# Optimization experiments

Measured on AMD Instinct MI355X. Metric: run time of the kernel, lower is better.

The kernel has to match this reference:

```python
import jax, jax.numpy as jnp
import numpy as np
import math

B, N, DIM, H, D = 2, 2048, 1024, 16, 64
EXPECTED_K = 1.0
LAYERSCALE_INIT = 0.001
EPS = 1e-6  # flax LayerNorm default


def layer_norm(x, scale, bias):
    mu = jnp.mean(x, axis=-1, keepdims=True)
    var = jnp.mean((x - mu) ** 2, axis=-1, keepdims=True)
    return (x - mu) * jax.lax.rsqrt(var + EPS) * scale + bias


def setup_inputs() -> dict:
    key = jax.random.key(0)
    ks = jax.random.split(key, 8)
    s = DIM ** -0.5
    x = jax.random.normal(ks[0], (B, N, DIM), jnp.float32)
    Wq = jax.random.normal(ks[1], (DIM, H * D), jnp.float32) * s
    Wk = jax.random.normal(ks[2], (DIM, H * D), jnp.float32) * s
    Wv = jax.random.normal(ks[3], (DIM, H * D), jnp.float32) * s
    Wo = jax.random.normal(ks[4], (H * D, DIM), jnp.float32) * ((H * D) ** -0.5)
    e = EXPECTED_K / N
    init_bias = jnp.full((1, 1, 1, 1), math.log(e / (1.0 - e)), jnp.float32)
    return {
        'x': x,
        'Wq': Wq, 'bq': jnp.zeros((H * D,), jnp.float32),
        'Wk': Wk, 'bk': jnp.zeros((H * D,), jnp.float32),
        'Wv': Wv, 'bv': jnp.zeros((H * D,), jnp.float32),
        'qn_scale': jnp.ones((D,), jnp.float32), 'qn_bias': jnp.zeros((D,), jnp.float32),
        'kn_scale': jnp.ones((D,), jnp.float32), 'kn_bias': jnp.zeros((D,), jnp.float32),
        'init_bias': init_bias,
        'Wo': Wo, 'bo': jnp.zeros((DIM,), jnp.float32),
        'gamma': jnp.full((DIM,), LAYERSCALE_INIT, jnp.float32),
    }


def reference(x, Wq, bq, Wk, bk, Wv, bv, qn_scale, qn_bias, kn_scale, kn_bias,
              init_bias, Wo, bo, gamma):
    Bv, Nv, _ = x.shape
    q = (x @ Wq + bq).reshape(Bv, Nv, H, D)
    k = (x @ Wk + bk).reshape(Bv, Nv, H, D)
    v = (x @ Wv + bv).reshape(Bv, Nv, H, D)
    q = layer_norm(q, qn_scale, qn_bias)
    k = layer_norm(k, kn_scale, kn_bias)
    q = jnp.swapaxes(q, 1, 2)  # [B,H,N,D]
    k = jnp.swapaxes(k, 1, 2)
    v = jnp.swapaxes(v, 1, 2)
    # NOTE: original code computes scale = head_dim**-0.5 but never applies it.
    attn_logits = jnp.einsum('bhid,bhjd->bhij', q, k)
    attn_weights = jax.nn.sigmoid(attn_logits + init_bias)
    out = jnp.einsum('bhij,bhjd->bhid', attn_weights, v)
    out = jnp.swapaxes(out, 1, 2).reshape(Bv, Nv, H * D)
    out = out @ Wo + bo
    return out * gamma
```

## Files before the change

kernel.cpp:

```cpp
#include <hip/hip_runtime.h>

#define DEV static __device__ __forceinline__

typedef __bf16 bf16x8 __attribute__((ext_vector_type(8)));
typedef __bf16 bf16x4 __attribute__((ext_vector_type(4)));
typedef float f32x4 __attribute__((ext_vector_type(4)));
typedef float f32x16 __attribute__((ext_vector_type(16)));
typedef unsigned int uint4v __attribute__((ext_vector_type(4)));
typedef unsigned short ushort4v __attribute__((ext_vector_type(4)));
using u16 = unsigned short;

#define NN 2048
#define DIMD 1024

DEV u16 f2bf(float f) {
    __bf16 b = (__bf16)f;
    return __builtin_bit_cast(u16, b);
}
DEV float bf2f(u16 s) {
    unsigned u = ((unsigned)s) << 16;
    return __builtin_bit_cast(float, u);
}
DEV bf16x8 load16(const u16* p) { return __builtin_bit_cast(bf16x8, *(const uint4v*)p); }
DEV f32x4 mfma16(bf16x8 a, bf16x8 b, f32x4 c) {
    return __builtin_amdgcn_mfma_f32_16x16x32_bf16(a, b, c, 0, 0, 0);
}
DEV f32x16 mfma32(bf16x8 a, bf16x8 b, f32x16 c) {
    return __builtin_amdgcn_mfma_f32_32x32x16_bf16(a, b, c, 0, 0, 0);
}
DEV void gl_lds16(const u16* g, u16* l) {
    __builtin_amdgcn_global_load_lds((const __attribute__((address_space(1))) void*)g,
                                     (__attribute__((address_space(3))) void*)l, 16, 0, 0);
}


__global__ __launch_bounds__(256) void k_prep(const float* __restrict__ x,
                                              const float* __restrict__ s0,
                                              const float* __restrict__ s1,
                                              const float* __restrict__ s2,
                                              const float* __restrict__ s3,
                                              u16* __restrict__ xb,
                                              u16* __restrict__ wqkv_t,
                                              u16* __restrict__ wo_t) {
    __shared__ float tile[32][33];
    const int z = blockIdx.z;
    if (z < 4) {
        const float* src = (z == 0) ? s0 : (z == 1) ? s1 : (z == 2) ? s2 : s3;
        u16* dst = (z < 3) ? (wqkv_t + (size_t)z * 1024 * 1024) : wo_t;
        int tx = threadIdx.x & 31, ty = threadIdx.x >> 5;
        int kb = blockIdx.y * 32, nb = blockIdx.x * 32;
#pragma unroll
        for (int j = 0; j < 4; ++j)
            tile[ty + 8 * j][tx] = src[(size_t)(kb + ty + 8 * j) * 1024 + nb + tx];
        __syncthreads();
#pragma unroll
        for (int j = 0; j < 4; ++j)
            dst[(size_t)(nb + ty + 8 * j) * 1024 + kb + tx] = f2bf(tile[tx][ty + 8 * j]);
    } else {
        const int bidx = blockIdx.y * 32 + blockIdx.x;
#pragma unroll
        for (int q = 0; q < 4; ++q) {
            int i = bidx * 1024 + q * 256 + threadIdx.x;
            float4 v = ((const float4*)x)[i];
            ushort4v o;
            o[0] = f2bf(v.x); o[1] = f2bf(v.y); o[2] = f2bf(v.z); o[3] = f2bf(v.w);
            *(ushort4v*)(xb + (size_t)i * 4) = o;
        }
    }
}

__global__ __launch_bounds__(256) void k_gemm_qkv(const u16* __restrict__ A,
                                                  const u16* __restrict__ Bt,
                                                  const float* __restrict__ bq,
                                                  const float* __restrict__ bk,
                                                  const float* __restrict__ bv,
                                                  const float* __restrict__ qs,
                                                  const float* __restrict__ qb,
                                                  const float* __restrict__ ks,
                                                  const float* __restrict__ kb_,
                                                  u16* __restrict__ Qf,
                                                  u16* __restrict__ Kf,
                                                  u16* __restrict__ Vf) {
    __shared__ u16 As[128 * 32];
    __shared__ u16 Bs[128 * 32];
    const int K = 1024;
    const int m0 = blockIdx.x * 128, n0 = blockIdx.y * 128;
    const int tid = threadIdx.x;
    const int lane = tid & 63, w = tid >> 6;
    const int wr = w >> 1, wc = w & 1;
    const int li = lane & 15, g = lane >> 4;

    f32x4 acc[4][4] = {};

    const u16* gA = A + (size_t)(m0 + w * 16 + (lane >> 2)) * K + (lane & 3) * 8;
    const u16* gB = Bt + (size_t)(n0 + w * 16 + (lane >> 2)) * K + (lane & 3) * 8;
    u16* lA = &As[(w * 16) * 32];
    u16* lB = &Bs[(w * 16) * 32];

    for (int k0 = 0; k0 < K; k0 += 32) {
        __syncthreads();
        gl_lds16(gA + k0, lA);
        gl_lds16(gA + (size_t)64 * K + k0, lA + 64 * 32);
        gl_lds16(gB + k0, lB);
        gl_lds16(gB + (size_t)64 * K + k0, lB + 64 * 32);
        asm volatile("s_waitcnt vmcnt(0)" ::: "memory");
        __syncthreads();
        bf16x8 af[4], bfv[4];
#pragma unroll
        for (int mi = 0; mi < 4; ++mi)
            af[mi] = load16(&As[(wr * 64 + mi * 16 + li) * 32 + g * 8]);
#pragma unroll
        for (int ni = 0; ni < 4; ++ni)
            bfv[ni] = load16(&Bs[(wc * 64 + ni * 16 + li) * 32 + g * 8]);
#pragma unroll
        for (int mi = 0; mi < 4; ++mi)
#pragma unroll
            for (int ni = 0; ni < 4; ++ni)
                acc[mi][ni] = mfma16(af[mi], bfv[ni], acc[mi][ni]);
    }

    const int col0 = n0 + wc * 64;
    const int seg = col0 >> 10;
    const int hcol = col0 & 1023;
    const int h = hcol >> 6;

    if (seg < 2) {
        const float* S = (seg == 0) ? qs : ks;
        const float* Bb = (seg == 0) ? qb : kb_;
        const float* bias = (seg == 0) ? bq : bk;
        u16* dst = (seg == 0) ? Qf : Kf;
        const float sc = (seg == 0) ? -1.44269504f : 1.0f;
        float lnS[4], lnB[4], bv4[4];
#pragma unroll
        for (int ni = 0; ni < 4; ++ni) {
            int d = ni * 16 + li;
            lnS[ni] = S[d] * sc; lnB[ni] = Bb[d] * sc; bv4[ni] = bias[hcol + d];
        }
#pragma unroll
        for (int mi = 0; mi < 4; ++mi) {
#pragma unroll
            for (int r = 0; r < 4; ++r) {
                float v0 = acc[mi][0][r] + bv4[0];
                float v1 = acc[mi][1][r] + bv4[1];
                float v2 = acc[mi][2][r] + bv4[2];
                float v3 = acc[mi][3][r] + bv4[3];
                float s1 = v0 + v1 + v2 + v3;
                float s2 = v0 * v0 + v1 * v1 + v2 * v2 + v3 * v3;
#pragma unroll
                for (int o = 1; o < 16; o <<= 1) {
                    s1 += __shfl_xor(s1, o);
                    s2 += __shfl_xor(s2, o);
                }
                float mu = s1 * (1.0f / 64.0f);
                float var = s2 * (1.0f / 64.0f) - mu * mu;
                float rsv = rsqrtf(var + 1e-6f);
                int row = m0 + wr * 64 + mi * 16 + 4 * g + r;
                int bseq = row >> 11, n = row & 2047;
                size_t base = ((size_t)(bseq * 16 + h)) * 131072 +
                              ((size_t)(n >> 5) * 4) * 512 + (size_t)(n & 31) * 8 +
                              (li >> 3) * 256 + (li & 7);
                dst[base + 0 * 512] = f2bf((v0 - mu) * rsv * lnS[0] + lnB[0]);
                dst[base + 1 * 512] = f2bf((v1 - mu) * rsv * lnS[1] + lnB[1]);
                dst[base + 2 * 512] = f2bf((v2 - mu) * rsv * lnS[2] + lnB[2]);
                dst[base + 3 * 512] = f2bf((v3 - mu) * rsv * lnS[3] + lnB[3]);
            }
        }
    } else {
        float bv4[4];
#pragma unroll
        for (int ni = 0; ni < 4; ++ni) bv4[ni] = bv[hcol + ni * 16 + li];
#pragma unroll
        for (int mi = 0; mi < 4; ++mi) {
#pragma unroll
            for (int r = 0; r < 4; ++r) {
                int row = m0 + wr * 64 + mi * 16 + 4 * g + r;
                int bseq = row >> 11, j = row & 2047;
                size_t vb_ = ((size_t)(bseq * 16 + h)) * 131072 +
                             ((size_t)((j >> 5) * 4 + ((j >> 4) & 1))) * 512 +
                             (size_t)(((j >> 3) & 1) * 32) * 8 + (j & 7);
#pragma unroll
                for (int ni = 0; ni < 4; ++ni)
                    Vf[vb_ + (ni >> 1) * 1024 + ((ni & 1) * 16 + li) * 8] =
                        f2bf(acc[mi][ni][r] + bv4[ni]);
            }
        }
    }
}

__global__ __launch_bounds__(256) void k_gemm_out(const u16* __restrict__ A,
                                                  const u16* __restrict__ Bt,
                                                  const float* __restrict__ bias,
                                                  const float* __restrict__ gamma,
                                                  float* __restrict__ out) {
    __shared__ u16 As[128 * 32];
    __shared__ u16 Bs[64 * 32];
    const int K = 1024, ldc = 1024;
    const int m0 = blockIdx.x * 128, n0 = blockIdx.y * 64;
    const int tid = threadIdx.x;
    const int lane = tid & 63, w = tid >> 6;
    const int wr = w >> 1, wc = w & 1;
    const int li = lane & 15, g = lane >> 4;

    f32x4 acc[4][2] = {};

    const u16* gA = A + (size_t)(m0 + w * 16 + (lane >> 2)) * K + (lane & 3) * 8;
    const u16* gB = Bt + (size_t)(n0 + w * 16 + (lane >> 2)) * K + (lane & 3) * 8;
    u16* lA = &As[(w * 16) * 32];
    u16* lB = &Bs[(w * 16) * 32];

    for (int k0 = 0; k0 < K; k0 += 32) {
        __syncthreads();
        gl_lds16(gA + k0, lA);
        gl_lds16(gA + (size_t)64 * K + k0, lA + 64 * 32);
        gl_lds16(gB + k0, lB);
        asm volatile("s_waitcnt vmcnt(0)" ::: "memory");
        __syncthreads();
        bf16x8 af[4], bfv[2];
#pragma unroll
        for (int mi = 0; mi < 4; ++mi)
            af[mi] = load16(&As[(wr * 64 + mi * 16 + li) * 32 + g * 8]);
#pragma unroll
        for (int ni = 0; ni < 2; ++ni)
            bfv[ni] = load16(&Bs[(wc * 32 + ni * 16 + li) * 32 + g * 8]);
#pragma unroll
        for (int mi = 0; mi < 4; ++mi)
#pragma unroll
            for (int ni = 0; ni < 2; ++ni)
                acc[mi][ni] = mfma16(af[mi], bfv[ni], acc[mi][ni]);
    }

#pragma unroll
    for (int mi = 0; mi < 4; ++mi) {
        int row = m0 + wr * 64 + mi * 16 + 4 * g;
#pragma unroll
        for (int ni = 0; ni < 2; ++ni) {
            int col = n0 + wc * 32 + ni * 16 + li;
            float bv_ = bias[col], gv = gamma[col];
            f32x4 v = acc[mi][ni];
#pragma unroll
            for (int r = 0; r < 4; ++r)
                out[(size_t)(row + r) * ldc + col] = (v[r] + bv_) * gv;
        }
    }
}

__global__ __launch_bounds__(256, 2) void k_attn(const u16* __restrict__ Qf,
                                                 const u16* __restrict__ Kf,
                                                 const u16* __restrict__ Vf,
                                                 const float* __restrict__ ib,
                                                 u16* __restrict__ attn_out) {
    __shared__ float red[2][64][65];
    const int bid = blockIdx.x;
    const int xcd = bid & 7, idx = bid >> 3;
    const int bh = xcd * 4 + (idx >> 5);
    const int iblk = idx & 31;
    const int b = bh >> 4, h = bh & 15;
    const int tid = threadIdx.x;
    const int jq = tid >> 6, lane = tid & 63;
    const int l32 = lane & 31, hi = lane >> 5;
    const float c0 = -ib[0] * 1.44269504f;
    const u16* Qb = Qf + (size_t)bh * 131072;
    const u16* Kb = Kf + (size_t)bh * 131072;
    const u16* Vb = Vf + (size_t)bh * 131072;
    const int it0 = iblk * 2;

    bf16x8 qf[2][4];
#pragma unroll
    for (int t = 0; t < 2; ++t)
#pragma unroll
        for (int s = 0; s < 4; ++s)
            qf[t][s] = load16(Qb + ((size_t)((it0 + t) * 4 + s)) * 512 + lane * 8);

    f32x16 accO[2][2] = {};
    const u16* kb0 = Kb + (size_t)(jq * 16) * 2048;
    const u16* vb0 = Vb + (size_t)(jq * 16) * 2048;

    f32x16 cinit;
#pragma unroll
    for (int r = 0; r < 16; ++r) cinit[r] = c0;

    bf16x8 kf[2][4];
#pragma unroll
    for (int s = 0; s < 4; ++s) kf[0][s] = load16(kb0 + s * 512 + lane * 8);
#pragma unroll
    for (int s = 0; s < 4; ++s) kf[1][s] = load16(kb0 + 2048 + s * 512 + lane * 8);
    f32x16 sa0 = cinit, sa1;
#pragma unroll
    for (int s = 0; s < 4; ++s) sa0 = mfma32(kf[0][s], qf[0][s], sa0);

#pragma unroll 2
    for (int jt = 0; jt < 16; ++jt) {
        const int cur = jt & 1, nxt = cur ^ 1;
        bf16x8 vf[2][2];
        const u16* vbc = vb0 + (size_t)jt * 2048;
#pragma unroll
        for (int db = 0; db < 2; ++db)
#pragma unroll
            for (int js = 0; js < 2; ++js)
                vf[db][js] = load16(vbc + (db * 2 + js) * 512 + lane * 8);
        __builtin_amdgcn_s_setprio(1);
        sa1 = cinit;
#pragma unroll
        for (int s = 0; s < 4; ++s) sa1 = mfma32(kf[cur][s], qf[1][s], sa1);
        __builtin_amdgcn_s_setprio(0);
        if (jt < 14) {
            const u16* kbn = kb0 + (size_t)(jt + 2) * 2048;
#pragma unroll
            for (int s = 0; s < 4; ++s) kf[cur][s] = load16(kbn + s * 512 + lane * 8);
        }
        __builtin_amdgcn_sched_barrier(0);
        bf16x8 p00, p01;
        {
            float p[16];
#pragma unroll
            for (int r = 0; r < 16; ++r) {
                float e = __builtin_amdgcn_exp2f(sa0[r]);
                p[r] = __builtin_amdgcn_rcpf(1.0f + e);
            }
            unsigned wd[8];
#pragma unroll
            for (int u2 = 0; u2 < 8; ++u2) {
                unsigned r_;
                asm("v_cvt_pk_bf16_f32 %0, %1, %2"
                    : "=v"(r_) : "v"(p[2 * u2]), "v"(p[2 * u2 + 1]));
                wd[u2] = r_;
            }
            asm("v_permlane32_swap_b32 %0, %1" : "+v"(wd[0]), "+v"(wd[2]));
            asm("v_permlane32_swap_b32 %0, %1" : "+v"(wd[1]), "+v"(wd[3]));
            asm("v_permlane32_swap_b32 %0, %1" : "+v"(wd[4]), "+v"(wd[6]));
            asm("v_permlane32_swap_b32 %0, %1" : "+v"(wd[5]), "+v"(wd[7]));
            uint4v u0 = {wd[0], wd[1], wd[2], wd[3]};
            uint4v u1 = {wd[4], wd[5], wd[6], wd[7]};
            p00 = __builtin_bit_cast(bf16x8, u0);
            p01 = __builtin_bit_cast(bf16x8, u1);
        }
        __builtin_amdgcn_sched_barrier(0);
        __builtin_amdgcn_s_setprio(1);
        accO[0][0] = mfma32(vf[0][0], p00, accO[0][0]);
        accO[0][0] = mfma32(vf[0][1], p01, accO[0][0]);
        accO[0][1] = mfma32(vf[1][0], p00, accO[0][1]);
        accO[0][1] = mfma32(vf[1][1], p01, accO[0][1]);
        if (jt < 15) {
            sa0 = cinit;
#pragma unroll
            for (int s = 0; s < 4; ++s) sa0 = mfma32(kf[nxt][s], qf[0][s], sa0);
        }
        __builtin_amdgcn_s_setprio(0);
        __builtin_amdgcn_sched_barrier(0);
        bf16x8 p10, p11;
        {
            float p[16];
#pragma unroll
            for (int r = 0; r < 16; ++r) {
                float e = __builtin_amdgcn_exp2f(sa1[r]);
                p[r] = __builtin_amdgcn_rcpf(1.0f + e);
            }
            unsigned wd[8];
#pragma unroll
            for (int u2 = 0; u2 < 8; ++u2) {
                unsigned r_;
                asm("v_cvt_pk_bf16_f32 %0, %1, %2"
                    : "=v"(r_) : "v"(p[2 * u2]), "v"(p[2 * u2 + 1]));
                wd[u2] = r_;
            }
            asm("v_permlane32_swap_b32 %0, %1" : "+v"(wd[0]), "+v"(wd[2]));
            asm("v_permlane32_swap_b32 %0, %1" : "+v"(wd[1]), "+v"(wd[3]));
            asm("v_permlane32_swap_b32 %0, %1" : "+v"(wd[4]), "+v"(wd[6]));
            asm("v_permlane32_swap_b32 %0, %1" : "+v"(wd[5]), "+v"(wd[7]));
            uint4v u0 = {wd[0], wd[1], wd[2], wd[3]};
            uint4v u1 = {wd[4], wd[5], wd[6], wd[7]};
            p10 = __builtin_bit_cast(bf16x8, u0);
            p11 = __builtin_bit_cast(bf16x8, u1);
        }
        __builtin_amdgcn_sched_barrier(0);
        __builtin_amdgcn_s_setprio(1);
        accO[1][0] = mfma32(vf[0][0], p10, accO[1][0]);
        accO[1][0] = mfma32(vf[0][1], p11, accO[1][0]);
        accO[1][1] = mfma32(vf[1][0], p10, accO[1][1]);
        accO[1][1] = mfma32(vf[1][1], p11, accO[1][1]);
        __builtin_amdgcn_s_setprio(0);
    }

    if (jq & 1) {
#pragma unroll
        for (int t = 0; t < 2; ++t)
#pragma unroll
            for (int db = 0; db < 2; ++db)
#pragma unroll
                for (int r = 0; r < 16; ++r)
                    red[jq >> 1][t * 32 + l32][db * 32 + (r & 3) + 8 * (r >> 2) + 4 * hi] =
                        accO[t][db][r];
    }
    __syncthreads();
    if (!(jq & 1)) {
#pragma unroll
        for (int t = 0; t < 2; ++t)
#pragma unroll
            for (int db = 0; db < 2; ++db)
#pragma unroll
                for (int r = 0; r < 16; ++r)
                    accO[t][db][r] +=
                        red[jq >> 1][t * 32 + l32][db * 32 + (r & 3) + 8 * (r >> 2) + 4 * hi];
    }
    __syncthreads();
    if (jq == 2) {
#pragma unroll
        for (int t = 0; t < 2; ++t)
#pragma unroll
            for (int db = 0; db < 2; ++db)
#pragma unroll
                for (int r = 0; r < 16; ++r)
                    red[0][t * 32 + l32][db * 32 + (r & 3) + 8 * (r >> 2) + 4 * hi] =
                        accO[t][db][r];
    }
    __syncthreads();
    if (jq == 0) {
#pragma unroll
        for (int t = 0; t < 2; ++t)
#pragma unroll
            for (int db = 0; db < 2; ++db)
#pragma unroll
                for (int r = 0; r < 16; ++r)
                    accO[t][db][r] +=
                        red[0][t * 32 + l32][db * 32 + (r & 3) + 8 * (r >> 2) + 4 * hi];
#pragma unroll
        for (int t = 0; t < 2; ++t) {
            const int i = it0 * 32 + t * 32 + l32;
#pragma unroll
            for (int db = 0; db < 2; ++db)
#pragma unroll
                for (int q = 0; q < 4; ++q) {
                    int d = db * 32 + 8 * q + 4 * hi;
                    bf16x4 o4;
#pragma unroll
                    for (int r = 0; r < 4; ++r) o4[r] = (__bf16)accO[t][db][4 * q + r];
                    *(bf16x4*)&attn_out[(size_t)(b * NN + i) * 1024 + h * 64 + d] = o4;
                }
        }
    }
}


extern "C" void kernel_launch(void* const* d_in, const int* in_sizes, int n_in,
                              void* d_out, int out_size, void* d_ws, size_t ws_size,
                              hipStream_t stream) {
    (void)in_sizes; (void)n_in; (void)out_size; (void)ws_size;
    const float* x     = (const float*)d_in[0];
    const float* Wq    = (const float*)d_in[1];
    const float* bq    = (const float*)d_in[2];
    const float* Wk    = (const float*)d_in[3];
    const float* bk    = (const float*)d_in[4];
    const float* Wv    = (const float*)d_in[5];
    const float* bv    = (const float*)d_in[6];
    const float* qn_s  = (const float*)d_in[7];
    const float* qn_b  = (const float*)d_in[8];
    const float* kn_s  = (const float*)d_in[9];
    const float* kn_b  = (const float*)d_in[10];
    const float* ib    = (const float*)d_in[11];
    const float* Wo    = (const float*)d_in[12];
    const float* bo    = (const float*)d_in[13];
    const float* gamma = (const float*)d_in[14];
    float* out = (float*)d_out;

    char* ws = (char*)d_ws;
    size_t off = 0;
    auto alloc = [&](size_t bytes) -> void* {
        void* p = ws + off;
        off += (bytes + 255) & ~(size_t)255;
        return p;
    };
    u16* xb       = (u16*)alloc((size_t)4096 * 1024 * 2);
    u16* wqkv_t   = (u16*)alloc((size_t)3072 * 1024 * 2);
    u16* wo_t     = (u16*)alloc((size_t)1024 * 1024 * 2);
    u16* Qf       = (u16*)alloc((size_t)32 * 131072 * 2);
    u16* Kf       = (u16*)alloc((size_t)32 * 131072 * 2);
    u16* Vf       = (u16*)alloc((size_t)32 * 131072 * 2);
    u16* attn_out = (u16*)alloc((size_t)4096 * 1024 * 2);

    k_prep<<<dim3(32, 32, 5), 256, 0, stream>>>(x, Wq, Wk, Wv, Wo, xb, wqkv_t, wo_t);
    k_gemm_qkv<<<dim3(32, 24), 256, 0, stream>>>(xb, wqkv_t, bq, bk, bv,
                                                 qn_s, qn_b, kn_s, kn_b, Qf, Kf, Vf);
    k_attn<<<1024, 256, 0, stream>>>(Qf, Kf, Vf, ib, attn_out);
    k_gemm_out<<<dim3(32, 16), 256, 0, stream>>>(attn_out, wo_t, bo, gamma, out);
}
```

Measured before the change: 121.1 us.

## Store GEMM operands in MFMA-fragment layout and load directly to registers

The prep kernel and the attention epilogue now write x, the weights and the attention output in a fragment-major tiled layout, so each lane can fetch its MFMA operand with one contiguous 16-byte global load. Both GEMMs drop LDS staging and barriers and instead double-buffer fragments in registers, prefetching the next K-step while the current one computes. This removes LDS traffic and syncs. In exchange, operand reuse across waves now relies on L2 rather than LDS, and register pressure rises. The sched_barriers in the attention loop are also removed, leaving instruction scheduling to the compiler.

```diff
diff --git a/kernel.cpp b/kernel.cpp
--- a/kernel.cpp
+++ b/kernel.cpp
@@ -28,9 +28,10 @@
 DEV f32x16 mfma32(bf16x8 a, bf16x8 b, f32x16 c) {
     return __builtin_amdgcn_mfma_f32_32x32x16_bf16(a, b, c, 0, 0, 0);
 }
-DEV void gl_lds16(const u16* g, u16* l) {
-    __builtin_amdgcn_global_load_lds((const __attribute__((address_space(1))) void*)g,
-                                     (__attribute__((address_space(3))) void*)l, 16, 0, 0);
+
+DEV size_t fslot(int row, int k) {
+    return ((size_t)((row >> 4) * 32 + (k >> 5)) << 9) + (size_t)(((k >> 3) & 3) << 7) +
+           (size_t)((row & 15) << 3) + (size_t)(k & 7);
 }
 
 
@@ -39,14 +40,14 @@
                                               const float* __restrict__ s1,
                                               const float* __restrict__ s2,
                                               const float* __restrict__ s3,
-                                              u16* __restrict__ xb,
-                                              u16* __restrict__ wqkv_t,
-                                              u16* __restrict__ wo_t) {
+                                              u16* __restrict__ xbf,
+                                              u16* __restrict__ wqkvf,
+                                              u16* __restrict__ wof) {
     __shared__ float tile[32][33];
     const int z = blockIdx.z;
     if (z < 4) {
         const float* src = (z == 0) ? s0 : (z == 1) ? s1 : (z == 2) ? s2 : s3;
-        u16* dst = (z < 3) ? (wqkv_t + (size_t)z * 1024 * 1024) : wo_t;
+        u16* dst = (z < 3) ? (wqkvf + (size_t)z * 1024 * 1024) : wof;
         int tx = threadIdx.x & 31, ty = threadIdx.x >> 5;
         int kb = blockIdx.y * 32, nb = blockIdx.x * 32;
 #pragma unroll
@@ -55,7 +56,7 @@
         __syncthreads();
 #pragma unroll
         for (int j = 0; j < 4; ++j)
-            dst[(size_t)(nb + ty + 8 * j) * 1024 + kb + tx] = f2bf(tile[tx][ty + 8 * j]);
+            dst[fslot(nb + ty + 8 * j, kb + tx)] = f2bf(tile[tx][ty + 8 * j]);
     } else {
         const int bidx = blockIdx.y * 32 + blockIdx.x;
 #pragma unroll
@@ -64,13 +65,15 @@
             float4 v = ((const float4*)x)[i];
             ushort4v o;
             o[0] = f2bf(v.x); o[1] = f2bf(v.y); o[2] = f2bf(v.z); o[3] = f2bf(v.w);
-            *(ushort4v*)(xb + (size_t)i * 4) = o;
-        }
-    }
-}
-
-__global__ __launch_bounds__(256) void k_gemm_qkv(const u16* __restrict__ A,
-                                                  const u16* __restrict__ Bt,
+            int row = i >> 8;
+            int k0 = (i * 4) & 1023;
+            *(ushort4v*)(xbf + fslot(row, k0)) = o;
+        }
+    }
+}
+
+__global__ __launch_bounds__(256) void k_gemm_qkv(const u16* __restrict__ Af,
+                                                  const u16* __restrict__ Bf,
                                                   const float* __restrict__ bq,
                                                   const float* __restrict__ bk,
                                                   const float* __restrict__ bv,
@@ -81,9 +84,6 @@
                                                   u16* __restrict__ Qf,
                                                   u16* __restrict__ Kf,
                                                   u16* __restrict__ Vf) {
-    __shared__ u16 As[128 * 32];
-    __shared__ u16 Bs[128 * 32];
-    const int K = 1024;
     const int m0 = blockIdx.x * 128, n0 = blockIdx.y * 128;
     const int tid = threadIdx.x;
     const int lane = tid & 63, w = tid >> 6;
@@ -92,31 +92,43 @@
 
     f32x4 acc[4][4] = {};
 
-    const u16* gA = A + (size_t)(m0 + w * 16 + (lane >> 2)) * K + (lane & 3) * 8;
-    const u16* gB = Bt + (size_t)(n0 + w * 16 + (lane >> 2)) * K + (lane & 3) * 8;
-    u16* lA = &As[(w * 16) * 32];
-    u16* lB = &Bs[(w * 16) * 32];
-
-    for (int k0 = 0; k0 < K; k0 += 32) {
-        __syncthreads();
-        gl_lds16(gA + k0, lA);
-        gl_lds16(gA + (size_t)64 * K + k0, lA + 64 * 32);
-        gl_lds16(gB + k0, lB);
-        gl_lds16(gB + (size_t)64 * K + k0, lB + 64 * 32);
-        asm volatile("s_waitcnt vmcnt(0)" ::: "memory");
-        __syncthreads();
-        bf16x8 af[4], bfv[4];
+    const u16* Ap[4];
+    const u16* Bp[4];
+#pragma unroll
+    for (int mi = 0; mi < 4; ++mi)
+        Ap[mi] = Af + (((size_t)((m0 >> 4) + wr * 4 + mi) * 32) << 9) + lane * 8;
+#pragma unroll
+    for (int ni = 0; ni < 4; ++ni)
+        Bp[ni] = Bf + (((size_t)((n0 >> 4) + wc * 4 + ni) * 32) << 9) + lane * 8;
+
+    bf16x8 Fa[2][4][2], Fb[2][4][2];
+#pragma unroll
+    for (int mi = 0; mi < 4; ++mi)
+#pragma unroll
+        for (int s = 0; s < 2; ++s) {
+            Fa[0][mi][s] = load16(Ap[mi] + (s << 9));
+            Fb[0][mi][s] = load16(Bp[mi] + (s << 9));
+        }
+
+#pragma unroll
+    for (int t = 0; t < 16; ++t) {
+        const int cur = t & 1, nxt = cur ^ 1;
+        if (t < 15) {
+#pragma unroll
+            for (int mi = 0; mi < 4; ++mi)
+#pragma unroll
+                for (int s = 0; s < 2; ++s) {
+                    Fa[nxt][mi][s] = load16(Ap[mi] + (((t + 1) * 2 + s) << 9));
+                    Fb[nxt][mi][s] = load16(Bp[mi] + (((t + 1) * 2 + s) << 9));
+                }
+        }
 #pragma unroll
         for (int mi = 0; mi < 4; ++mi)
-            af[mi] = load16(&As[(wr * 64 + mi * 16 + li) * 32 + g * 8]);
-#pragma unroll
-        for (int ni = 0; ni < 4; ++ni)
-            bfv[ni] = load16(&Bs[(wc * 64 + ni * 16 + li) * 32 + g * 8]);
-#pragma unroll
-        for (int mi = 0; mi < 4; ++mi)
-#pragma unroll
-            for (int ni = 0; ni < 4; ++ni)
-                acc[mi][ni] = mfma16(af[mi], bfv[ni], acc[mi][ni]);
+#pragma unroll
+            for (int ni = 0; ni < 4; ++ni) {
+                acc[mi][ni] = mfma16(Fa[cur][mi][0], Fb[cur][ni][0], acc[mi][ni]);
+                acc[mi][ni] = mfma16(Fa[cur][mi][1], Fb[cur][ni][1], acc[mi][ni]);
+            }
     }
 
     const int col0 = n0 + wc * 64;
@@ -187,14 +199,12 @@
     }
 }
 
-__global__ __launch_bounds__(256) void k_gemm_out(const u16* __restrict__ A,
-                                                  const u16* __restrict__ Bt,
+__global__ __launch_bounds__(256) void k_gemm_out(const u16* __restrict__ Af,
+                                                  const u16* __restrict__ Bf,
                                                   const float* __restrict__ bias,
                                                   const float* __restrict__ gamma,
                                                   float* __restrict__ out) {
-    __shared__ u16 As[128 * 32];
-    __shared__ u16 Bs[64 * 32];
-    const int K = 1024, ldc = 1024;
+    const int ldc = 1024;
     const int m0 = blockIdx.x * 128, n0 = blockIdx.y * 64;
     const int tid = threadIdx.x;
     const int lane = tid & 63, w = tid >> 6;
@@ -203,30 +213,47 @@
 
     f32x4 acc[4][2] = {};
 
-    const u16* gA = A + (size_t)(m0 + w * 16 + (lane >> 2)) * K + (lane & 3) * 8;
-    const u16* gB = Bt + (size_t)(n0 + w * 16 + (lane >> 2)) * K + (lane & 3) * 8;
-    u16* lA = &As[(w * 16) * 32];
-    u16* lB = &Bs[(w * 16) * 32];
-
-    for (int k0 = 0; k0 < K; k0 += 32) {
-        __syncthreads();
-        gl_lds16(gA + k0, lA);
-        gl_lds16(gA + (size_t)64 * K + k0, lA + 64 * 32);
-        gl_lds16(gB + k0, lB);
-        asm volatile("s_waitcnt vmcnt(0)" ::: "memory");
-        __syncthreads();
-        bf16x8 af[4], bfv[2];
+    const u16* Ap[4];
+    const u16* Bp[2];
+#pragma unroll
+    for (int mi = 0; mi < 4; ++mi)
+        Ap[mi] = Af + (((size_t)((m0 >> 4) + wr * 4 + mi) * 32) << 9) + lane * 8;
+#pragma unroll
+    for (int ni = 0; ni < 2; ++ni)
+        Bp[ni] = Bf + (((size_t)((n0 >> 4) + wc * 2 + ni) * 32) << 9) + lane * 8;
+
+    bf16x8 Fa[2][4][2], Fb[2][2][2];
+#pragma unroll
+    for (int mi = 0; mi < 4; ++mi)
+#pragma unroll
+        for (int s = 0; s < 2; ++s) Fa[0][mi][s] = load16(Ap[mi] + (s << 9));
+#pragma unroll
+    for (int ni = 0; ni < 2; ++ni)
+#pragma unroll
+        for (int s = 0; s < 2; ++s) Fb[0][ni][s] = load16(Bp[ni] + (s << 9));
+
+#pragma unroll
+    for (int t = 0; t < 16; ++t) {
+        const int cur = t & 1, nxt = cur ^ 1;
+        if (t < 15) {
+#pragma unroll
+            for (int mi = 0; mi < 4; ++mi)
+#pragma unroll
+                for (int s = 0; s < 2; ++s)
+                    Fa[nxt][mi][s] = load16(Ap[mi] + (((t + 1) * 2 + s) << 9));
+#pragma unroll
+            for (int ni = 0; ni < 2; ++ni)
+#pragma unroll
+                for (int s = 0; s < 2; ++s)
+                    Fb[nxt][ni][s] = load16(Bp[ni] + (((t + 1) * 2 + s) << 9));
+        }
 #pragma unroll
         for (int mi = 0; mi < 4; ++mi)
-            af[mi] = load16(&As[(wr * 64 + mi * 16 + li) * 32 + g * 8]);
-#pragma unroll
-        for (int ni = 0; ni < 2; ++ni)
-            bfv[ni] = load16(&Bs[(wc * 32 + ni * 16 + li) * 32 + g * 8]);
-#pragma unroll
-        for (int mi = 0; mi < 4; ++mi)
-#pragma unroll
-            for (int ni = 0; ni < 2; ++ni)
-                acc[mi][ni] = mfma16(af[mi], bfv[ni], acc[mi][ni]);
+#pragma unroll
+            for (int ni = 0; ni < 2; ++ni) {
+                acc[mi][ni] = mfma16(Fa[cur][mi][0], Fb[cur][ni][0], acc[mi][ni]);
+                acc[mi][ni] = mfma16(Fa[cur][mi][1], Fb[cur][ni][1], acc[mi][ni]);
+            }
     }
 
 #pragma unroll
@@ -308,7 +335,6 @@
 #pragma unroll
             for (int s = 0; s < 4; ++s) kf[cur][s] = load16(kbn + s * 512 + lane * 8);
         }
-        __builtin_amdgcn_sched_barrier(0);
         bf16x8 p00, p01;
         {
             float p[16];
@@ -334,7 +360,6 @@
             p00 = __builtin_bit_cast(bf16x8, u0);
             p01 = __builtin_bit_cast(bf16x8, u1);
         }
-        __builtin_amdgcn_sched_barrier(0);
         __builtin_amdgcn_s_setprio(1);
         accO[0][0] = mfma32(vf[0][0], p00, accO[0][0]);
         accO[0][0] = mfma32(vf[0][1], p01, accO[0][0]);
@@ -346,7 +371,6 @@
             for (int s = 0; s < 4; ++s) sa0 = mfma32(kf[nxt][s], qf[0][s], sa0);
         }
         __builtin_amdgcn_s_setprio(0);
-        __builtin_amdgcn_sched_barrier(0);
         bf16x8 p10, p11;
         {
             float p[16];
@@ -372,7 +396,6 @@
             p10 = __builtin_bit_cast(bf16x8, u0);
             p11 = __builtin_bit_cast(bf16x8, u1);
         }
-        __builtin_amdgcn_sched_barrier(0);
         __builtin_amdgcn_s_setprio(1);
         accO[1][0] = mfma32(vf[0][0], p10, accO[1][0]);
         accO[1][0] = mfma32(vf[0][1], p11, accO[1][0]);
@@ -426,15 +449,16 @@
 #pragma unroll
         for (int t = 0; t < 2; ++t) {
             const int i = it0 * 32 + t * 32 + l32;
+            const size_t rowpart = ((size_t)((b * 128 + (i >> 4)) * 32 + h * 2)) << 9;
 #pragma unroll
             for (int db = 0; db < 2; ++db)
 #pragma unroll
                 for (int q = 0; q < 4; ++q) {
-                    int d = db * 32 + 8 * q + 4 * hi;
                     bf16x4 o4;
 #pragma unroll
                     for (int r = 0; r < 4; ++r) o4[r] = (__bf16)accO[t][db][4 * q + r];
-                    *(bf16x4*)&attn_out[(size_t)(b * NN + i) * 1024 + h * 64 + d] = o4;
+                    size_t slot = rowpart + ((size_t)db << 9) + (q << 7) + ((i & 15) << 3) + 4 * hi;
+                    *(bf16x4*)&attn_out[slot] = o4;
                 }
         }
     }
@@ -469,17 +493,17 @@
         off += (bytes + 255) & ~(size_t)255;
         return p;
     };
-    u16* xb       = (u16*)alloc((size_t)4096 * 1024 * 2);
-    u16* wqkv_t   = (u16*)alloc((size_t)3072 * 1024 * 2);
-    u16* wo_t     = (u16*)alloc((size_t)1024 * 1024 * 2);
+    u16* xbf      = (u16*)alloc((size_t)4096 * 1024 * 2);
+    u16* wqkvf    = (u16*)alloc((size_t)3072 * 1024 * 2);
+    u16* wof      = (u16*)alloc((size_t)1024 * 1024 * 2);
     u16* Qf       = (u16*)alloc((size_t)32 * 131072 * 2);
     u16* Kf       = (u16*)alloc((size_t)32 * 131072 * 2);
     u16* Vf       = (u16*)alloc((size_t)32 * 131072 * 2);
     u16* attn_out = (u16*)alloc((size_t)4096 * 1024 * 2);
 
-    k_prep<<<dim3(32, 32, 5), 256, 0, stream>>>(x, Wq, Wk, Wv, Wo, xb, wqkv_t, wo_t);
-    k_gemm_qkv<<<dim3(32, 24), 256, 0, stream>>>(xb, wqkv_t, bq, bk, bv,
+    k_prep<<<dim3(32, 32, 5), 256, 0, stream>>>(x, Wq, Wk, Wv, Wo, xbf, wqkvf, wof);
+    k_gemm_qkv<<<dim3(32, 24), 256, 0, stream>>>(xbf, wqkvf, bq, bk, bv,
                                                  qn_s, qn_b, kn_s, kn_b, Qf, Kf, Vf);
     k_attn<<<1024, 256, 0, stream>>>(Qf, Kf, Vf, ib, attn_out);
-    k_gemm_out<<<dim3(32, 16), 256, 0, stream>>>(attn_out, wo_t, bo, gamma, out);
-}
+    k_gemm_out<<<dim3(32, 16), 256, 0, stream>>>(attn_out, wof, bo, gamma, out);
+}
```

Measured after the change: 152.2 us. 25.6% more time.
